# Optimization experiments

Hardware: AMD Instinct MI355X
Metric: run time of the kernel (lower is better)

The kernel has to match this reference:

```python
import jax, jax.numpy as jnp
import numpy as np

B, H, S, D = 4, 12, 2048, 64


def setup_inputs() -> dict:
    key = jax.random.key(0)
    k1, k2, k3 = jax.random.split(key, 3)
    keys = jax.random.normal(k1, (B, H, S, D), dtype=jnp.float32)
    queries = jax.random.normal(k2, (B, H, S, D), dtype=jnp.float32)
    values = jax.random.normal(k3, (B, H, S, D), dtype=jnp.float32)
    return {"keys": keys, "queries": queries, "values": values}


def reference(keys, queries, values):
    d_k = keys.shape[-1]
    # scores: [B, H, S, S]
    scores = jnp.einsum("bhqd,bhkd->bhqk", queries, keys) / jnp.sqrt(jnp.asarray(d_k, dtype=scores_dtype(queries)))
    s = scores.shape[-1]
    causal = jnp.triu(jnp.ones((s, s), dtype=bool), k=1)  # True above diagonal -> masked
    scores = jnp.where(causal, -jnp.inf, scores)
    attn = jax.nn.softmax(scores, axis=-1)
    return jnp.einsum("bhqk,bhkd->bhqd", attn, values)


def scores_dtype(x):
    return x.dtype
```

## Files before the change

kernel.cpp:

```cpp
#include <hip/hip_runtime.h>
#include <hip/hip_bf16.h>

#define B_SZ 4
#define H_SZ 12
#define S_LEN 2048
#define DH 64
#define KT 64
#define NQT (S_LEN / 64)
#define PK 72
#define M2 9.0f

typedef _Float16 half8 __attribute__((ext_vector_type(8)));
typedef _Float16 half4v __attribute__((ext_vector_type(4)));
typedef float f32x4 __attribute__((ext_vector_type(4)));

__global__ __launch_bounds__(256, 3) void fa_fwd(
    const float* __restrict__ Kg,
    const float* __restrict__ Qg,
    const float* __restrict__ Vg,
    float* __restrict__ Og)
{
    const int bh = blockIdx.x;
    const int j  = blockIdx.y;
    const size_t base = (size_t)bh * S_LEN * DH;

    const int tid  = threadIdx.x;
    const int wave = tid >> 6;
    const int lane = tid & 63;
    const int l16  = lane & 15;
    const int quad = lane >> 4;

    __shared__ __align__(16) _Float16 Klds[2][KT * PK];
    __shared__ __align__(16) _Float16 Vlds[2][DH * 64];

    const int rlo = j * 64 + wave * 16;
    const int rhi = (NQT - 1 - j) * 64 + wave * 16;

    const float qs = 0.125f * 1.44269504f;
    half8 qlo[2], qhi[2];
    {
        const float* plo = Qg + base + (size_t)(rlo + l16) * DH + quad * 8;
        const float* phi = Qg + base + (size_t)(rhi + l16) * DH + quad * 8;
#pragma unroll
        for (int c = 0; c < 2; ++c) {
            float4 x = *(const float4*)(plo + c * 32);
            float4 y = *(const float4*)(plo + c * 32 + 4);
            half8 f;
            f[0]=(_Float16)(x.x*qs); f[1]=(_Float16)(x.y*qs); f[2]=(_Float16)(x.z*qs); f[3]=(_Float16)(x.w*qs);
            f[4]=(_Float16)(y.x*qs); f[5]=(_Float16)(y.y*qs); f[6]=(_Float16)(y.z*qs); f[7]=(_Float16)(y.w*qs);
            qlo[c] = f;
            x = *(const float4*)(phi + c * 32);
            y = *(const float4*)(phi + c * 32 + 4);
            f[0]=(_Float16)(x.x*qs); f[1]=(_Float16)(x.y*qs); f[2]=(_Float16)(x.z*qs); f[3]=(_Float16)(x.w*qs);
            f[4]=(_Float16)(y.x*qs); f[5]=(_Float16)(y.y*qs); f[6]=(_Float16)(y.z*qs); f[7]=(_Float16)(y.w*qs);
            qhi[c] = f;
        }
    }

    float4 kreg[4];
    float  vreg[16];

    auto load_tile = [&](int kv0) {
#pragma unroll
        for (int i = 0; i < 4; ++i) {
            int f = tid + 256 * i;
            kreg[i] = *(const float4*)(Kg + base + (size_t)(kv0 + (f >> 4)) * DH + ((f & 15) << 2));
        }
        const float* vp = Vg + base + (size_t)(kv0 + wave * 16) * DH + lane;
#pragma unroll
        for (int jj = 0; jj < 16; ++jj) vreg[jj] = vp[jj * DH];
    };
    auto cvt_store = [&](int b) {
#pragma unroll
        for (int i = 0; i < 4; ++i) {
            int f = tid + 256 * i;
            half4v hk = {(_Float16)kreg[i].x, (_Float16)kreg[i].y,
                         (_Float16)kreg[i].z, (_Float16)kreg[i].w};
            *(half4v*)&Klds[b][(f >> 4) * PK + ((f & 15) << 2)] = hk;
        }
        half8 lo, hi;
#pragma unroll
        for (int jj = 0; jj < 8; ++jj) { lo[jj] = (_Float16)vreg[jj]; hi[jj] = (_Float16)vreg[jj + 8]; }
        _Float16* vrow = &Vlds[b][lane * 64];
        *(half8*)&vrow[(((2 * wave + 0) ^ (lane & 7)) << 3)] = lo;
        *(half8*)&vrow[(((2 * wave + 1) ^ (lane & 7)) << 3)] = hi;
    };

    f32x4 olo[4], ohi[4];
#pragma unroll
    for (int t = 0; t < 4; ++t) { olo[t] = f32x4{0.f,0.f,0.f,0.f}; ohi[t] = f32x4{0.f,0.f,0.f,0.f}; }
    f32x4 llo = f32x4{0.f,0.f,0.f,0.f}, lhi = f32x4{0.f,0.f,0.f,0.f};
    const half8 ones = {(_Float16)1.f,(_Float16)1.f,(_Float16)1.f,(_Float16)1.f,
                        (_Float16)1.f,(_Float16)1.f,(_Float16)1.f,(_Float16)1.f};

    const int kr0    = ((l16 >> 2) << 3) + (l16 & 3);
    const int qrow64 = wave * 16 + l16;
    const int klq    = quad * 8;

    auto kfrag = [&](int b, int c, int t) -> half8 {
        return *(const half8*)&Klds[b][(kr0 + ((t & 1) << 2) + ((t >> 1) << 5)) * PK + c * 32 + quad * 8];
    };
    auto vfrag = [&](int b, int c, int t) -> half8 {
        int d = l16 + 16 * t;
        return *(const half8*)&Vlds[b][d * 64 + ((((c << 2) + quad) ^ (d & 7)) << 3)];
    };
    auto mask_diag = [&](f32x4* sc) {
#pragma unroll
        for (int t = 0; t < 4; ++t)
#pragma unroll
            for (int r = 0; r < 4; ++r)
                if (klq + ((t & 1) << 2) + ((t >> 1) << 5) + r > qrow64) sc[t][r] = -1e30f;
    };
    auto exp_all = [&](f32x4* sc) {
#pragma unroll
        for (int t = 0; t < 4; ++t)
#pragma unroll
            for (int r = 0; r < 4; ++r)
                sc[t][r] = __builtin_amdgcn_exp2f(sc[t][r] - M2);
    };
    auto pack_pa = [&](const f32x4* sc, int c) -> half8 {
        half8 pa;
        const f32x4 s0 = sc[2 * c], s1 = sc[2 * c + 1];
        pa[0] = (_Float16)s0[0]; pa[1] = (_Float16)s0[1];
        pa[2] = (_Float16)s0[2]; pa[3] = (_Float16)s0[3];
        pa[4] = (_Float16)s1[0]; pa[5] = (_Float16)s1[1];
        pa[6] = (_Float16)s1[2]; pa[7] = (_Float16)s1[3];
        return pa;
    };

    auto do_single = [&](int b, const half8* qf, f32x4* oacc, f32x4& lacc, bool diag) {
        f32x4 sc[4];
#pragma unroll
        for (int t = 0; t < 4; ++t) sc[t] = f32x4{0.f,0.f,0.f,0.f};
#pragma unroll
        for (int c = 0; c < 2; ++c)
#pragma unroll
            for (int t = 0; t < 4; ++t)
                sc[t] = __builtin_amdgcn_mfma_f32_16x16x32_f16(kfrag(b, c, t), qf[c], sc[t], 0, 0, 0);
        if (diag) mask_diag(sc);
        exp_all(sc);
#pragma unroll
        for (int c = 0; c < 2; ++c) {
            half8 pa = pack_pa(sc, c);
            lacc = __builtin_amdgcn_mfma_f32_16x16x32_f16(ones, pa, lacc, 0, 0, 0);
#pragma unroll
            for (int t = 0; t < 4; ++t)
                oacc[t] = __builtin_amdgcn_mfma_f32_16x16x32_f16(vfrag(b, c, t), pa, oacc[t], 0, 0, 0);
        }
    };

    auto do_dual = [&](int b, bool dlo) {
        f32x4 sh[4], sl[4];
#pragma unroll
        for (int t = 0; t < 4; ++t) { sh[t] = f32x4{0.f,0.f,0.f,0.f}; sl[t] = f32x4{0.f,0.f,0.f,0.f}; }
#pragma unroll
        for (int c = 0; c < 2; ++c)
#pragma unroll
            for (int t = 0; t < 4; ++t) {
                half8 kf = kfrag(b, c, t);
                sh[t] = __builtin_amdgcn_mfma_f32_16x16x32_f16(kf, qhi[c], sh[t], 0, 0, 0);
                sl[t] = __builtin_amdgcn_mfma_f32_16x16x32_f16(kf, qlo[c], sl[t], 0, 0, 0);
            }
        if (dlo) mask_diag(sl);
        exp_all(sh);
        exp_all(sl);
#pragma unroll
        for (int c = 0; c < 2; ++c) {
            half8 ph = pack_pa(sh, c);
            half8 pl = pack_pa(sl, c);
            lhi = __builtin_amdgcn_mfma_f32_16x16x32_f16(ones, ph, lhi, 0, 0, 0);
            llo = __builtin_amdgcn_mfma_f32_16x16x32_f16(ones, pl, llo, 0, 0, 0);
#pragma unroll
            for (int t = 0; t < 4; ++t) {
                half8 vb = vfrag(b, c, t);
                ohi[t] = __builtin_amdgcn_mfma_f32_16x16x32_f16(vb, ph, ohi[t], 0, 0, 0);
                olo[t] = __builtin_amdgcn_mfma_f32_16x16x32_f16(vb, pl, olo[t], 0, 0, 0);
            }
        }
    };

    const int niter = NQT - j;
    load_tile(0);
    int b = 0;
    for (int it = 0; it < niter; ++it) {
        cvt_store(b);
        __syncthreads();
        if (it + 1 < niter) load_tile((it + 1) * KT);
        asm volatile("" ::: "memory");
        if (it <= j) do_dual(b, it == j);
        else         do_single(b, qhi, ohi, lhi, it == niter - 1);
        b ^= 1;
    }

    const float il = 1.0f / llo[0];
    const float ih = 1.0f / lhi[0];
#pragma unroll
    for (int t = 0; t < 4; ++t) {
        *(f32x4*)(Og + base + (size_t)(rlo + l16) * DH + 16 * t + quad * 4) = olo[t] * il;
        *(f32x4*)(Og + base + (size_t)(rhi + l16) * DH + 16 * t + quad * 4) = ohi[t] * ih;
    }
}

extern "C" void kernel_launch(void* const* d_in, const int* in_sizes, int n_in,
                              void* d_out, int out_size, void* d_ws, size_t ws_size,
                              hipStream_t stream) {
    const float* K = (const float*)d_in[0];
    const float* Q = (const float*)d_in[1];
    const float* V = (const float*)d_in[2];
    float* O = (float*)d_out;
    dim3 grid(B_SZ * H_SZ, NQT / 2);
    fa_fwd<<<grid, dim3(256), 0, stream>>>(K, Q, V, O);
}
```

Measured before the change: 177.2 us.

## Pre-convert K/V to swizzled fp16 workspace and stream tiles via global_load_lds

Adds a pre-pass kernel that converts K and V to fp16 once, with V transposed and both written in a swizzled tile layout into the workspace. The attention kernel then copies tiles straight from global memory into LDS with global_load_lds, which removes the per-block conversion and register staging that were repeated for every query block. It also raises wave priority around the MFMA sections. The cost is an extra kernel launch and an extra write and read pass over K and V in fp16, and the new path only runs when a large enough workspace is provided.

```diff
diff --git a/kernel.cpp b/kernel.cpp
--- a/kernel.cpp
+++ b/kernel.cpp
@@ -14,10 +14,64 @@
 typedef _Float16 half4v __attribute__((ext_vector_type(4)));
 typedef float f32x4 __attribute__((ext_vector_type(4)));
 
-__global__ __launch_bounds__(256, 3) void fa_fwd(
-    const float* __restrict__ Kg,
+__device__ __forceinline__ int gk_swz(int row) { return ((row & 3) << 1) | ((row >> 3) & 1); }
+__device__ __forceinline__ int gv_swz(int d) { return (d & 7) ^ ((d >> 3) & 7); }
+
+#define GLOAD_LDS16(gp, lp)                                                              \
+    __builtin_amdgcn_global_load_lds(                                                    \
+        (const __attribute__((address_space(1))) void*)(gp),                             \
+        (__attribute__((address_space(3))) void*)(lp), 16, 0, 0)
+
+__global__ __launch_bounds__(256) void cvt_pre(
+    const float* __restrict__ Kg, const float* __restrict__ Vg,
+    _Float16* __restrict__ wsK, _Float16* __restrict__ wsV)
+{
+    const int blk = blockIdx.x;
+    const size_t gbase = (size_t)blk * (64 * 64);
+    const int t = threadIdx.x;
+
+    __shared__ float vt[64 * 65];
+
+#pragma unroll
+    for (int i = 0; i < 4; ++i) {
+        int f = t + 256 * i;
+        int row = f >> 4, c4 = (f & 15) << 2;
+        float4 v = *(const float4*)(Vg + gbase + row * 64 + c4);
+        vt[row * 65 + c4 + 0] = v.x; vt[row * 65 + c4 + 1] = v.y;
+        vt[row * 65 + c4 + 2] = v.z; vt[row * 65 + c4 + 3] = v.w;
+    }
+
+#pragma unroll
+    for (int i = 0; i < 2; ++i) {
+        int u = t + 256 * i;
+        int row = u >> 3, p = u & 7;
+        int s = p ^ gk_swz(row);
+        float4 x = *(const float4*)(Kg + gbase + row * 64 + s * 8);
+        float4 y = *(const float4*)(Kg + gbase + row * 64 + s * 8 + 4);
+        half8 h;
+        h[0]=(_Float16)x.x; h[1]=(_Float16)x.y; h[2]=(_Float16)x.z; h[3]=(_Float16)x.w;
+        h[4]=(_Float16)y.x; h[5]=(_Float16)y.y; h[6]=(_Float16)y.z; h[7]=(_Float16)y.w;
+        *(half8*)&wsK[(size_t)blk * 4096 + row * 64 + p * 8] = h;
+    }
+
+    __syncthreads();
+
+#pragma unroll
+    for (int i = 0; i < 2; ++i) {
+        int u = t + 256 * i;
+        int d = u >> 3, p = u & 7;
+        int s = p ^ gv_swz(d);
+        half8 h;
+#pragma unroll
+        for (int e = 0; e < 8; ++e) h[e] = (_Float16)vt[(s * 8 + e) * 65 + d];
+        *(half8*)&wsV[(size_t)blk * 4096 + d * 64 + p * 8] = h;
+    }
+}
+
+__global__ __launch_bounds__(256, 3) void fa_fwd_ws(
+    const _Float16* __restrict__ wsK,
+    const _Float16* __restrict__ wsV,
     const float* __restrict__ Qg,
-    const float* __restrict__ Vg,
     float* __restrict__ Og)
 {
     const int bh = blockIdx.x;
@@ -30,8 +84,8 @@
     const int l16  = lane & 15;
     const int quad = lane >> 4;
 
-    __shared__ __align__(16) _Float16 Klds[2][KT * PK];
-    __shared__ __align__(16) _Float16 Vlds[2][DH * 64];
+    __shared__ __align__(16) _Float16 Klds[2][64 * 64];
+    __shared__ __align__(16) _Float16 Vlds[2][64 * 64];
 
     const int rlo = j * 64 + wave * 16;
     const int rhi = (NQT - 1 - j) * 64 + wave * 16;
@@ -57,6 +111,186 @@
         }
     }
 
+    auto stage = [&](int bb, int tile) {
+        const size_t toff = ((size_t)(bh * 32 + tile)) << 13;
+        const char* kS = (const char*)wsK + toff + wave * 2048 + lane * 16;
+        const char* vS = (const char*)wsV + toff + wave * 2048 + lane * 16;
+        char* kL = (char*)&Klds[bb][0] + wave * 2048;
+        char* vL = (char*)&Vlds[bb][0] + wave * 2048;
+        GLOAD_LDS16(kS,        kL);
+        GLOAD_LDS16(kS + 1024, kL + 1024);
+        GLOAD_LDS16(vS,        vL);
+        GLOAD_LDS16(vS + 1024, vL + 1024);
+    };
+
+    f32x4 olo[4], ohi[4];
+#pragma unroll
+    for (int t = 0; t < 4; ++t) { olo[t] = f32x4{0.f,0.f,0.f,0.f}; ohi[t] = f32x4{0.f,0.f,0.f,0.f}; }
+    f32x4 llo = f32x4{0.f,0.f,0.f,0.f}, lhi = f32x4{0.f,0.f,0.f,0.f};
+    const half8 ones = {(_Float16)1.f,(_Float16)1.f,(_Float16)1.f,(_Float16)1.f,
+                        (_Float16)1.f,(_Float16)1.f,(_Float16)1.f,(_Float16)1.f};
+
+    const int kr0    = ((l16 >> 2) << 3) + (l16 & 3);
+    const int qrow64 = wave * 16 + l16;
+    const int klq    = quad * 8;
+
+    auto kfrag = [&](int b, int c, int t) -> half8 {
+        int row = kr0 + ((t & 1) << 2) + ((t >> 1) << 5);
+        int p = (((c << 2) + quad) ^ gk_swz(row));
+        return *(const half8*)&Klds[b][row * 64 + (p << 3)];
+    };
+    auto vfrag = [&](int b, int c, int t) -> half8 {
+        int d = l16 + 16 * t;
+        int p = (((c << 2) + quad) ^ gv_swz(d));
+        return *(const half8*)&Vlds[b][d * 64 + (p << 3)];
+    };
+    auto mask_diag = [&](f32x4* sc) {
+#pragma unroll
+        for (int t = 0; t < 4; ++t)
+#pragma unroll
+            for (int r = 0; r < 4; ++r)
+                if (klq + ((t & 1) << 2) + ((t >> 1) << 5) + r > qrow64) sc[t][r] = -1e30f;
+    };
+    auto exp_all = [&](f32x4* sc) {
+#pragma unroll
+        for (int t = 0; t < 4; ++t)
+#pragma unroll
+            for (int r = 0; r < 4; ++r)
+                sc[t][r] = __builtin_amdgcn_exp2f(sc[t][r] - M2);
+    };
+    auto pack_pa = [&](const f32x4* sc, int c) -> half8 {
+        half8 pa;
+        const f32x4 s0 = sc[2 * c], s1 = sc[2 * c + 1];
+        pa[0] = (_Float16)s0[0]; pa[1] = (_Float16)s0[1];
+        pa[2] = (_Float16)s0[2]; pa[3] = (_Float16)s0[3];
+        pa[4] = (_Float16)s1[0]; pa[5] = (_Float16)s1[1];
+        pa[6] = (_Float16)s1[2]; pa[7] = (_Float16)s1[3];
+        return pa;
+    };
+
+    auto do_single = [&](int b, const half8* qf, f32x4* oacc, f32x4& lacc, bool diag) {
+        f32x4 sc[4];
+#pragma unroll
+        for (int t = 0; t < 4; ++t) sc[t] = f32x4{0.f,0.f,0.f,0.f};
+        __builtin_amdgcn_s_setprio(1);
+#pragma unroll
+        for (int c = 0; c < 2; ++c)
+#pragma unroll
+            for (int t = 0; t < 4; ++t)
+                sc[t] = __builtin_amdgcn_mfma_f32_16x16x32_f16(kfrag(b, c, t), qf[c], sc[t], 0, 0, 0);
+        __builtin_amdgcn_s_setprio(0);
+        if (diag) mask_diag(sc);
+        exp_all(sc);
+#pragma unroll
+        for (int c = 0; c < 2; ++c) {
+            half8 pa = pack_pa(sc, c);
+            __builtin_amdgcn_s_setprio(1);
+            lacc = __builtin_amdgcn_mfma_f32_16x16x32_f16(ones, pa, lacc, 0, 0, 0);
+#pragma unroll
+            for (int t = 0; t < 4; ++t)
+                oacc[t] = __builtin_amdgcn_mfma_f32_16x16x32_f16(vfrag(b, c, t), pa, oacc[t], 0, 0, 0);
+            __builtin_amdgcn_s_setprio(0);
+        }
+    };
+
+    auto do_dual = [&](int b, bool dlo) {
+        f32x4 sh[4], sl[4];
+#pragma unroll
+        for (int t = 0; t < 4; ++t) { sh[t] = f32x4{0.f,0.f,0.f,0.f}; sl[t] = f32x4{0.f,0.f,0.f,0.f}; }
+        __builtin_amdgcn_s_setprio(1);
+#pragma unroll
+        for (int c = 0; c < 2; ++c)
+#pragma unroll
+            for (int t = 0; t < 4; ++t) {
+                half8 kf = kfrag(b, c, t);
+                sh[t] = __builtin_amdgcn_mfma_f32_16x16x32_f16(kf, qhi[c], sh[t], 0, 0, 0);
+                sl[t] = __builtin_amdgcn_mfma_f32_16x16x32_f16(kf, qlo[c], sl[t], 0, 0, 0);
+            }
+        __builtin_amdgcn_s_setprio(0);
+        if (dlo) mask_diag(sl);
+        exp_all(sh);
+        exp_all(sl);
+#pragma unroll
+        for (int c = 0; c < 2; ++c) {
+            half8 ph = pack_pa(sh, c);
+            half8 pl = pack_pa(sl, c);
+            __builtin_amdgcn_s_setprio(1);
+            lhi = __builtin_amdgcn_mfma_f32_16x16x32_f16(ones, ph, lhi, 0, 0, 0);
+            llo = __builtin_amdgcn_mfma_f32_16x16x32_f16(ones, pl, llo, 0, 0, 0);
+#pragma unroll
+            for (int t = 0; t < 4; ++t) {
+                half8 vb = vfrag(b, c, t);
+                ohi[t] = __builtin_amdgcn_mfma_f32_16x16x32_f16(vb, ph, ohi[t], 0, 0, 0);
+                olo[t] = __builtin_amdgcn_mfma_f32_16x16x32_f16(vb, pl, olo[t], 0, 0, 0);
+            }
+            __builtin_amdgcn_s_setprio(0);
+        }
+    };
+
+    const int niter = NQT - j;
+    int b = 0;
+    stage(0, 0);
+    for (int it = 0; it < niter; ++it) {
+        __syncthreads();
+        if (it + 1 < niter) stage(b ^ 1, it + 1);
+        asm volatile("" ::: "memory");
+        if (it <= j) do_dual(b, it == j);
+        else         do_single(b, qhi, ohi, lhi, it == niter - 1);
+        b ^= 1;
+    }
+
+    const float il = 1.0f / llo[0];
+    const float ih = 1.0f / lhi[0];
+#pragma unroll
+    for (int t = 0; t < 4; ++t) {
+        *(f32x4*)(Og + base + (size_t)(rlo + l16) * DH + 16 * t + quad * 4) = olo[t] * il;
+        *(f32x4*)(Og + base + (size_t)(rhi + l16) * DH + 16 * t + quad * 4) = ohi[t] * ih;
+    }
+}
+
+__global__ __launch_bounds__(256, 3) void fa_fwd_legacy(
+    const float* __restrict__ Kg,
+    const float* __restrict__ Qg,
+    const float* __restrict__ Vg,
+    float* __restrict__ Og)
+{
+    const int bh = blockIdx.x;
+    const int j  = blockIdx.y;
+    const size_t base = (size_t)bh * S_LEN * DH;
+
+    const int tid  = threadIdx.x;
+    const int wave = tid >> 6;
+    const int lane = tid & 63;
+    const int l16  = lane & 15;
+    const int quad = lane >> 4;
+
+    __shared__ __align__(16) _Float16 Klds[2][KT * PK];
+    __shared__ __align__(16) _Float16 Vlds[2][DH * 64];
+
+    const int rlo = j * 64 + wave * 16;
+    const int rhi = (NQT - 1 - j) * 64 + wave * 16;
+
+    const float qs = 0.125f * 1.44269504f;
+    half8 qlo[2], qhi[2];
+    {
+        const float* plo = Qg + base + (size_t)(rlo + l16) * DH + quad * 8;
+        const float* phi = Qg + base + (size_t)(rhi + l16) * DH + quad * 8;
+#pragma unroll
+        for (int c = 0; c < 2; ++c) {
+            float4 x = *(const float4*)(plo + c * 32);
+            float4 y = *(const float4*)(plo + c * 32 + 4);
+            half8 f;
+            f[0]=(_Float16)(x.x*qs); f[1]=(_Float16)(x.y*qs); f[2]=(_Float16)(x.z*qs); f[3]=(_Float16)(x.w*qs);
+            f[4]=(_Float16)(y.x*qs); f[5]=(_Float16)(y.y*qs); f[6]=(_Float16)(y.z*qs); f[7]=(_Float16)(y.w*qs);
+            qlo[c] = f;
+            x = *(const float4*)(phi + c * 32);
+            y = *(const float4*)(phi + c * 32 + 4);
+            f[0]=(_Float16)(x.x*qs); f[1]=(_Float16)(x.y*qs); f[2]=(_Float16)(x.z*qs); f[3]=(_Float16)(x.w*qs);
+            f[4]=(_Float16)(y.x*qs); f[5]=(_Float16)(y.y*qs); f[6]=(_Float16)(y.z*qs); f[7]=(_Float16)(y.w*qs);
+            qhi[c] = f;
+        }
+    }
+
     float4 kreg[4];
     float  vreg[16];
 
@@ -208,6 +442,18 @@
     const float* Q = (const float*)d_in[1];
     const float* V = (const float*)d_in[2];
     float* O = (float*)d_out;
-    dim3 grid(B_SZ * H_SZ, NQT / 2);
-    fa_fwd<<<grid, dim3(256), 0, stream>>>(K, Q, V, O);
+
+    const size_t halfs_per_tensor = (size_t)B_SZ * H_SZ * S_LEN * DH;
+    const size_t ws_needed = 2 * halfs_per_tensor * sizeof(_Float16);
+
+    if (d_ws != nullptr && ws_size >= ws_needed) {
+        _Float16* wsK = (_Float16*)d_ws;
+        _Float16* wsV = wsK + halfs_per_tensor;
+        cvt_pre<<<dim3(B_SZ * H_SZ * NQT), dim3(256), 0, stream>>>(K, V, wsK, wsV);
+        dim3 grid(B_SZ * H_SZ, NQT / 2);
+        fa_fwd_ws<<<grid, dim3(256), 0, stream>>>(wsK, wsV, Q, O);
+    } else {
+        dim3 grid(B_SZ * H_SZ, NQT / 2);
+        fa_fwd_legacy<<<grid, dim3(256), 0, stream>>>(K, Q, V, O);
+    }
 }
```

After: 149.7 us. -15.5%, faster.
